# Performance work log

Measured on AMD Instinct MI355X. Metric: run time of the kernel, lower is better.

Reference implementation:

```python
import jax, jax.numpy as jnp
import numpy as np

N_NODES = 50000

def gcn_conv(x, W, b, row, col, ew, n):
    # PyG GCNConv: linear first (no bias in lin), then gcn_norm with added
    # self-loops (weight 1.0), symmetric D^{-1/2} normalization, scatter-add
    # aggregation from row (source) to col (target), then bias.
    h = x @ W                                      # [N, out]
    loop = jnp.arange(n, dtype=row.dtype)
    row_f = jnp.concatenate([row, loop])
    col_f = jnp.concatenate([col, loop])
    ew_f = jnp.concatenate([ew, jnp.ones((n,), dtype=ew.dtype)])
    deg = jax.ops.segment_sum(ew_f, col_f, num_segments=n)
    dinv = jnp.where(deg > 0, jax.lax.rsqrt(jnp.maximum(deg, 1e-30)), 0.0)
    norm = dinv[row_f] * ew_f * dinv[col_f]        # [E+N]
    msg = norm[:, None] * h[row_f]                 # gather + scale
    out = jax.ops.segment_sum(msg, col_f, num_segments=n)  # scatter-add
    return out + b

def setup_inputs() -> dict:
    key = jax.random.key(0)
    k = jax.random.split(key, 8)
    in_dim, hidden_dim, out_dim = 128, 256, 128
    n, e = N_NODES, 600000
    x = jax.random.normal(k[0], (n, in_dim), dtype=jnp.float32)
    edge_index = jax.random.randint(k[1], (2, e), 0, n, dtype=jnp.int64)
    edge_weight = jax.random.uniform(k[2], (e,), dtype=jnp.float32)
    # Glorot-style params (PyG GCNConv lin has no bias; bias added after aggregation)
    W1 = jax.random.normal(k[3], (in_dim, hidden_dim), dtype=jnp.float32) / np.sqrt(in_dim)
    b1 = jnp.zeros((hidden_dim,), dtype=jnp.float32)
    W2 = jax.random.normal(k[4], (hidden_dim, out_dim), dtype=jnp.float32) / np.sqrt(hidden_dim)
    b2 = jnp.zeros((out_dim,), dtype=jnp.float32)
    return {"x": x, "edge_index": edge_index, "edge_weight": edge_weight,
            "W1": W1, "b1": b1, "W2": W2, "b2": b2}

def reference(x, edge_index, edge_weight, W1, b1, W2, b2):
    n = x.shape[0]
    row, col = edge_index[0], edge_index[1]
    h = jax.nn.relu(gcn_conv(x, W1, b1, row, col, edge_weight, n))
    # dropout is identity in eval mode
    out = jax.nn.relu(gcn_conv(h, W2, b2, row, col, edge_weight, n))
    return out
```

## Files before the change

kernel.cpp:

```cpp
#include <hip/hip_runtime.h>
#include <hip/hip_bf16.h>

constexpr int IN_DIM  = 128;
constexpr int HID     = 256;
constexpr int OUT_DIM = 128;
constexpr int ELL_W   = 64;

typedef __attribute__((ext_vector_type(8))) short short8;
typedef __attribute__((ext_vector_type(8))) unsigned short ushort8;
typedef __attribute__((ext_vector_type(4))) float f32x4;

__device__ __forceinline__ float bf2f(unsigned short u) {
    return __uint_as_float(((unsigned int)u) << 16);
}
__device__ __forceinline__ unsigned short f2bf(float f) {
    unsigned int u = __float_as_uint(f);
    u += 0x7FFFu + ((u >> 16) & 1u);
    return (unsigned short)(u >> 16);
}
__device__ __forceinline__ unsigned short f2h(float f) {
    _Float16 h = (_Float16)f;
    unsigned short b;
    __builtin_memcpy(&b, &h, 2);
    return b;
}
__device__ __forceinline__ float h2f(unsigned short b) {
    _Float16 h;
    __builtin_memcpy(&h, &b, 2);
    return (float)h;
}
__device__ __forceinline__ unsigned int pack_e(int src, float w) {
    return (unsigned int)src | ((unsigned int)f2h(w) << 16);
}

__global__ void k_prep(int* __restrict__ cnt, int n,
                       const float* __restrict__ W1, unsigned short* __restrict__ w1t,
                       const float* __restrict__ W2, unsigned short* __restrict__ w2t) {
    const int i = blockIdx.x * 256 + threadIdx.x;
    if (i < n) cnt[i] = 0;
    if (i < IN_DIM * HID) {
        const int k = i / HID, nn = i % HID;
        w1t[(size_t)nn * IN_DIM + k] = f2bf(W1[i]);
    }
    if (i < HID * OUT_DIM) {
        const int k = i / OUT_DIM, nn = i % OUT_DIM;
        w2t[(size_t)nn * HID + k] = f2bf(W2[i]);
    }
}

__global__ void k_fill_ell(const int* __restrict__ row, const int* __restrict__ col,
                           const float* __restrict__ ew, int* __restrict__ cnt,
                           unsigned int* __restrict__ ell, int E) {
    const int e = blockIdx.x * blockDim.x + threadIdx.x;
    if (e < E) {
        const int c = col[e];
        const int p = atomicAdd(&cnt[c], 1);
        if (p < ELL_W)
            __builtin_nontemporal_store(pack_e(row[e], ew[e]), &ell[(size_t)c * ELL_W + p]);
    }
}

__global__ __launch_bounds__(256)
void k_deg_xs(const int* __restrict__ cnt, const unsigned int* __restrict__ ell,
              const float* __restrict__ x, float* __restrict__ dinv,
              unsigned short* __restrict__ xs, int n) {
    const int wave = threadIdx.x >> 6;
    const int lane = threadIdx.x & 63;
    const int node = blockIdx.x * 4 + wave;
    if (node >= n) return;
    const int m = min(cnt[node], ELL_W);
    float s = (lane < m) ? h2f((unsigned short)(ell[(size_t)node * ELL_W + lane] >> 16)) : 0.f;
    #pragma unroll
    for (int d = 32; d; d >>= 1) s += __shfl_xor(s, d);
    const float di = rsqrtf(1.0f + s);
    if (lane == 0) dinv[node] = di;
    const float2 v = *reinterpret_cast<const float2*>(x + (size_t)node * IN_DIM + lane * 2);
    const unsigned int packed = (unsigned int)f2bf(v.x * di) |
                                ((unsigned int)f2bf(v.y * di) << 16);
    *reinterpret_cast<unsigned int*>(xs + (size_t)node * IN_DIM + lane * 2) = packed;
}

template<bool BIAS_RELU, bool BF16OUT>
__global__ __launch_bounds__(256)
void k_gather_w(const int* __restrict__ cnt, const unsigned int* __restrict__ ell,
                const float* __restrict__ dinv, const unsigned short* __restrict__ hs,
                const float* __restrict__ bias, void* __restrict__ out_, int n) {
    constexpr int F = 128;
    const int gid  = threadIdx.x >> 4;
    const int gw   = gid & 3;
    const int l16  = threadIdx.x & 15;
    const int j8   = l16 * 8;
    const int node = blockIdx.x * 16 + gid;
    if (node >= n) return;

    const int m = min(cnt[node], ELL_W);
    const unsigned int* bucket = ell + (size_t)node * ELL_W;

    const float dc = dinv[node];
    const ushort8 hv = *reinterpret_cast<const ushort8*>(hs + (size_t)node * F + j8);

    float acc[8] = {};
    for (int base = 0; base < m; base += 16) {
        const unsigned int mt = (base + l16 < m) ? bucket[base + l16] : 0u;
        const int c16   = min(m - base, 16);
        const int quads = (c16 + 3) >> 2;
        unsigned int u[4];
        ushort8 v[4];
        #pragma unroll
        for (int i = 0; i < 4; ++i) {
            u[i] = __shfl(mt, gw * 16 + i);
            v[i] = *(const ushort8*)&hs[(size_t)(u[i] & 0xFFFFu) * F + j8];
        }
        for (int q = 1; q < quads; ++q) {
            unsigned int nu[4];
            ushort8 nv[4];
            #pragma unroll
            for (int i = 0; i < 4; ++i) {
                nu[i] = __shfl(mt, gw * 16 + q * 4 + i);
                nv[i] = *(const ushort8*)&hs[(size_t)(nu[i] & 0xFFFFu) * F + j8];
            }
            #pragma unroll
            for (int i = 0; i < 4; ++i) {
                const float f = h2f((unsigned short)(u[i] >> 16));
                #pragma unroll
                for (int k = 0; k < 8; ++k) acc[k] = fmaf(f, bf2f(v[i][k]), acc[k]);
            }
            #pragma unroll
            for (int i = 0; i < 4; ++i) { u[i] = nu[i]; v[i] = nv[i]; }
        }
        #pragma unroll
        for (int i = 0; i < 4; ++i) {
            const float f = h2f((unsigned short)(u[i] >> 16));
            #pragma unroll
            for (int k = 0; k < 8; ++k) acc[k] = fmaf(f, bf2f(v[i][k]), acc[k]);
        }
    }

    float o[8];
    if (BIAS_RELU) {
        const float4 b0 = *reinterpret_cast<const float4*>(bias + j8);
        const float4 b1 = *reinterpret_cast<const float4*>(bias + j8 + 4);
        const float bb[8] = {b0.x, b0.y, b0.z, b0.w, b1.x, b1.y, b1.z, b1.w};
        #pragma unroll
        for (int i = 0; i < 8; ++i)
            o[i] = fmaxf(fmaf(dc, acc[i] + bf2f(hv[i]), bb[i]), 0.f);
    } else {
        #pragma unroll
        for (int i = 0; i < 8; ++i) o[i] = dc * (acc[i] + bf2f(hv[i]));
    }
    if (BF16OUT) {
        unsigned short ob[8];
        #pragma unroll
        for (int i = 0; i < 8; ++i) ob[i] = f2bf(o[i]);
        *reinterpret_cast<uint4*>((unsigned short*)out_ + (size_t)node * F + j8) =
            *reinterpret_cast<uint4*>(ob);
    } else {
        float* op = (float*)out_ + (size_t)node * F + j8;
        *reinterpret_cast<float4*>(op)     = make_float4(o[0], o[1], o[2], o[3]);
        *reinterpret_cast<float4*>(op + 4) = make_float4(o[4], o[5], o[6], o[7]);
    }
}

__global__ __launch_bounds__(256, 2)
void k_gemm_fused(const unsigned short* __restrict__ A,
                  const unsigned short* __restrict__ W1t,
                  const unsigned short* __restrict__ W2t,
                  const float* __restrict__ b1,
                  const float* __restrict__ dinv,
                  unsigned short* __restrict__ H2,
                  int n, int tpb) {
    __shared__ unsigned short As[2][32 * 128];
    __shared__ unsigned short Hs[32 * 256];
    __shared__ unsigned short Os[32 * 128];

    const int t    = threadIdx.x;
    const int w    = t >> 6;
    const int lane = t & 63;
    const int quad = lane >> 4;
    const int l16  = lane & 15;
    const int xr   = (l16 & 7) << 3;

    short8 bw1[4][4];
    #pragma unroll
    for (int nt = 0; nt < 4; ++nt)
        #pragma unroll
        for (int ks = 0; ks < 4; ++ks)
            bw1[nt][ks] = *(const short8*)&W1t[(size_t)(w * 64 + nt * 16 + l16) * 128 + ks * 32 + quad * 8];
    short8 bw2[2][8];
    #pragma unroll
    for (int nt = 0; nt < 2; ++nt)
        #pragma unroll
        for (int ks = 0; ks < 8; ++ks)
            bw2[nt][ks] = *(const short8*)&W2t[(size_t)(w * 32 + nt * 16 + l16) * 256 + ks * 32 + quad * 8];
    float bv[4];
    #pragma unroll
    for (int nt = 0; nt < 4; ++nt) bv[nt] = b1[w * 64 + nt * 16 + l16];

    const int tile0 = blockIdx.x * tpb;

    auto stage = [&](int buf, int tile) {
        #pragma unroll
        for (int j = 0; j < 2; ++j) {
            const int ci = j * 256 + t;
            const int r  = ci >> 4;
            const int c  = (ci & 15) ^ (r & 7);
            __builtin_amdgcn_global_load_lds(
                (const __attribute__((address_space(1))) uint32_t*)(A + ((size_t)tile * 32 + r) * 128 + c * 8),
                (__attribute__((address_space(3))) uint32_t*)(&As[buf][ci * 8]), 16, 0, 0);
        }
    };

    stage(0, tile0);
    __syncthreads();

    for (int it = 0; it < tpb; ++it) {
        const int tile = tile0 + it;
        if (it + 1 < tpb) stage((it + 1) & 1, tile + 1);

        f32x4 acc1[2][4] = {};
        #pragma unroll
        for (int ks = 0; ks < 4; ++ks) {
            short8 af[2];
            #pragma unroll
            for (int mt = 0; mt < 2; ++mt)
                af[mt] = *(const short8*)&As[it & 1][(mt * 16 + l16) * 128 + ((ks * 32 + quad * 8) ^ xr)];
            #pragma unroll
            for (int mt = 0; mt < 2; ++mt)
                #pragma unroll
                for (int nt = 0; nt < 4; ++nt)
                    acc1[mt][nt] = __builtin_amdgcn_mfma_f32_16x16x32_bf16(
                        af[mt], bw1[nt][ks], acc1[mt][nt], 0, 0, 0);
        }
        __syncthreads();

        #pragma unroll
        for (int mt = 0; mt < 2; ++mt)
            #pragma unroll
            for (int i = 0; i < 4; ++i) {
                const int r  = mt * 16 + quad * 4 + i;
                const int xw = (r & 7) << 3;
                #pragma unroll
                for (int nt = 0; nt < 4; ++nt) {
                    const int col = w * 64 + nt * 16 + l16;
                    Hs[r * 256 + (col ^ xw)] = f2bf(fmaxf(acc1[mt][nt][i] + bv[nt], 0.f));
                }
            }
        __syncthreads();

        f32x4 acc2[2][2] = {};
        #pragma unroll
        for (int ks = 0; ks < 8; ++ks) {
            short8 af[2];
            #pragma unroll
            for (int mt = 0; mt < 2; ++mt)
                af[mt] = *(const short8*)&Hs[(mt * 16 + l16) * 256 + ((ks * 32 + quad * 8) ^ xr)];
            #pragma unroll
            for (int mt = 0; mt < 2; ++mt)
                #pragma unroll
                for (int nt = 0; nt < 2; ++nt)
                    acc2[mt][nt] = __builtin_amdgcn_mfma_f32_16x16x32_bf16(
                        af[mt], bw2[nt][ks], acc2[mt][nt], 0, 0, 0);
        }

        #pragma unroll
        for (int mt = 0; mt < 2; ++mt)
            #pragma unroll
            for (int i = 0; i < 4; ++i) {
                const int r  = mt * 16 + quad * 4 + i;
                const int rg = tile * 32 + r;
                const float dr = (rg < n) ? dinv[rg] : 0.f;
                const int xw = (r & 7) << 3;
                #pragma unroll
                for (int nt = 0; nt < 2; ++nt) {
                    const int col = w * 32 + nt * 16 + l16;
                    Os[r * 128 + (col ^ xw)] = f2bf(acc2[mt][nt][i] * dr);
                }
            }
        __syncthreads();

        #pragma unroll
        for (int j = 0; j < 2; ++j) {
            const int ci = j * 256 + t;
            const int r  = ci >> 4;
            const int cr = ci & 15;
            *(uint4*)&H2[((size_t)tile * 32 + r) * 128 + cr * 8] =
                *(const uint4*)&Os[r * 128 + ((cr ^ (r & 7)) * 8)];
        }
    }
}

extern "C" void kernel_launch(void* const* d_in, const int* in_sizes, int n_in,
                              void* d_out, int out_size, void* d_ws, size_t ws_size,
                              hipStream_t stream) {
    const float* x  = (const float*)d_in[0];
    const int*   ei = (const int*)d_in[1];
    const float* ew = (const float*)d_in[2];
    const float* W1 = (const float*)d_in[3];
    const float* b1 = (const float*)d_in[4];
    const float* W2 = (const float*)d_in[5];
    const float* b2 = (const float*)d_in[6];
    float* out = (float*)d_out;

    const int n = in_sizes[0] / IN_DIM;
    const int E = in_sizes[1] / 2;
    const int Mpad = (n + 127) & ~127;
    const int ntiles = Mpad / 32;
    const int TPB = 4;
    const int* row = ei;
    const int* col = ei + E;

    float* ws = (float*)d_ws;
    size_t o = 0;
    auto alloc = [&](size_t words) { float* p = ws + o; o += (words + 63) & ~(size_t)63; return p; };
    float* dinv = alloc(n);
    int*   cnt  = (int*)alloc(n);
    unsigned int* ell = (unsigned int*)alloc((size_t)n * ELL_W);
    unsigned short* xs   = (unsigned short*)alloc((size_t)Mpad * IN_DIM / 2);
    unsigned short* aggx = (unsigned short*)alloc((size_t)Mpad * IN_DIM / 2);
    unsigned short* h2s  = (unsigned short*)alloc((size_t)Mpad * OUT_DIM / 2);
    unsigned short* w1t  = (unsigned short*)alloc((size_t)IN_DIM * HID / 2);
    unsigned short* w2t  = (unsigned short*)alloc((size_t)HID * OUT_DIM / 2);

    k_prep<<<(n + 255) / 256, 256, 0, stream>>>(cnt, n, W1, w1t, W2, w2t);
    k_fill_ell<<<(E + 255) / 256, 256, 0, stream>>>(row, col, ew, cnt, ell, E);
    k_deg_xs<<<(n + 3) / 4, 256, 0, stream>>>(cnt, ell, x, dinv, xs, n);

    k_gather_w<false, true><<<(n + 15) / 16, 256, 0, stream>>>(cnt, ell, dinv, xs, nullptr, aggx, n);

    k_gemm_fused<<<ntiles / TPB, 256, 0, stream>>>(aggx, w1t, w2t, b1, dinv, h2s, n, TPB);

    k_gather_w<true, false><<<(n + 15) / 16, 256, 0, stream>>>(cnt, ell, dinv, h2s, b2, out, n);
}
```

Measured before the change: 205.7 us.

## Split gather feature dimension into four slices with cross-lane edge reduction

The gather kernel now launches four blocks per node chunk, each handling a 32-feature slice. Within a 16-lane group, the lanes split into four edge sub-groups of four lanes, so each lane loads 16 bytes of a different edge's row, followed by a shuffle reduction. The aim is to get more independent memory requests in flight and better L2 locality per slice, at the cost of re-reading each ELL bucket four times and doing extra shuffles. The bucket load is also made nontemporal, and the GEMM tiles-per-block drops from 4 to 2 to launch more blocks.

```diff
diff --git a/kernel.cpp b/kernel.cpp
--- a/kernel.cpp
+++ b/kernel.cpp
@@ -82,82 +82,76 @@
 
 template<bool BIAS_RELU, bool BF16OUT>
 __global__ __launch_bounds__(256)
-void k_gather_w(const int* __restrict__ cnt, const unsigned int* __restrict__ ell,
-                const float* __restrict__ dinv, const unsigned short* __restrict__ hs,
-                const float* __restrict__ bias, void* __restrict__ out_, int n) {
+void k_gather_sl(const int* __restrict__ cnt, const unsigned int* __restrict__ ell,
+                 const float* __restrict__ dinv, const unsigned short* __restrict__ hs,
+                 const float* __restrict__ bias, void* __restrict__ out_, int n) {
     constexpr int F = 128;
+    const int slice = blockIdx.x & 3;
+    const int chunk = blockIdx.x >> 2;
     const int gid  = threadIdx.x >> 4;
     const int gw   = gid & 3;
     const int l16  = threadIdx.x & 15;
-    const int j8   = l16 * 8;
-    const int node = blockIdx.x * 16 + gid;
+    const int node = chunk * 16 + gid;
     if (node >= n) return;
+
+    const int sl = slice * 32;
+    const int fq = (l16 & 3) * 8;
+    const int eo = l16 >> 2;
 
     const int m = min(cnt[node], ELL_W);
     const unsigned int* bucket = ell + (size_t)node * ELL_W;
-
     const float dc = dinv[node];
-    const ushort8 hv = *reinterpret_cast<const ushort8*>(hs + (size_t)node * F + j8);
 
     float acc[8] = {};
     for (int base = 0; base < m; base += 16) {
-        const unsigned int mt = (base + l16 < m) ? bucket[base + l16] : 0u;
-        const int c16   = min(m - base, 16);
-        const int quads = (c16 + 3) >> 2;
+        const unsigned int mt = (base + l16 < m) ?
+            __builtin_nontemporal_load(bucket + base + l16) : 0u;
         unsigned int u[4];
         ushort8 v[4];
         #pragma unroll
-        for (int i = 0; i < 4; ++i) {
-            u[i] = __shfl(mt, gw * 16 + i);
-            v[i] = *(const ushort8*)&hs[(size_t)(u[i] & 0xFFFFu) * F + j8];
-        }
-        for (int q = 1; q < quads; ++q) {
-            unsigned int nu[4];
-            ushort8 nv[4];
-            #pragma unroll
-            for (int i = 0; i < 4; ++i) {
-                nu[i] = __shfl(mt, gw * 16 + q * 4 + i);
-                nv[i] = *(const ushort8*)&hs[(size_t)(nu[i] & 0xFFFFu) * F + j8];
-            }
-            #pragma unroll
-            for (int i = 0; i < 4; ++i) {
-                const float f = h2f((unsigned short)(u[i] >> 16));
-                #pragma unroll
-                for (int k = 0; k < 8; ++k) acc[k] = fmaf(f, bf2f(v[i][k]), acc[k]);
-            }
-            #pragma unroll
-            for (int i = 0; i < 4; ++i) { u[i] = nu[i]; v[i] = nv[i]; }
-        }
-        #pragma unroll
-        for (int i = 0; i < 4; ++i) {
-            const float f = h2f((unsigned short)(u[i] >> 16));
-            #pragma unroll
-            for (int k = 0; k < 8; ++k) acc[k] = fmaf(f, bf2f(v[i][k]), acc[k]);
-        }
-    }
-
-    float o[8];
-    if (BIAS_RELU) {
-        const float4 b0 = *reinterpret_cast<const float4*>(bias + j8);
-        const float4 b1 = *reinterpret_cast<const float4*>(bias + j8 + 4);
-        const float bb[8] = {b0.x, b0.y, b0.z, b0.w, b1.x, b1.y, b1.z, b1.w};
-        #pragma unroll
-        for (int i = 0; i < 8; ++i)
-            o[i] = fmaxf(fmaf(dc, acc[i] + bf2f(hv[i]), bb[i]), 0.f);
-    } else {
-        #pragma unroll
-        for (int i = 0; i < 8; ++i) o[i] = dc * (acc[i] + bf2f(hv[i]));
-    }
-    if (BF16OUT) {
-        unsigned short ob[8];
-        #pragma unroll
-        for (int i = 0; i < 8; ++i) ob[i] = f2bf(o[i]);
-        *reinterpret_cast<uint4*>((unsigned short*)out_ + (size_t)node * F + j8) =
-            *reinterpret_cast<uint4*>(ob);
-    } else {
-        float* op = (float*)out_ + (size_t)node * F + j8;
-        *reinterpret_cast<float4*>(op)     = make_float4(o[0], o[1], o[2], o[3]);
-        *reinterpret_cast<float4*>(op + 4) = make_float4(o[4], o[5], o[6], o[7]);
+        for (int s = 0; s < 4; ++s) {
+            u[s] = __shfl(mt, gw * 16 + s * 4 + eo);
+            v[s] = *(const ushort8*)&hs[(size_t)(u[s] & 0xFFFFu) * F + sl + fq];
+        }
+        #pragma unroll
+        for (int s = 0; s < 4; ++s) {
+            const float f = h2f((unsigned short)(u[s] >> 16));
+            #pragma unroll
+            for (int k = 0; k < 8; ++k) acc[k] = fmaf(f, bf2f(v[s][k]), acc[k]);
+        }
+    }
+
+    #pragma unroll
+    for (int k = 0; k < 8; ++k) {
+        acc[k] += __shfl_xor(acc[k], 4);
+        acc[k] += __shfl_xor(acc[k], 8);
+    }
+
+    if (l16 < 4) {
+        const ushort8 hv = *(const ushort8*)&hs[(size_t)node * F + sl + l16 * 8];
+        float o[8];
+        if (BIAS_RELU) {
+            const float4 b0 = *(const float4*)&bias[sl + l16 * 8];
+            const float4 b1 = *(const float4*)&bias[sl + l16 * 8 + 4];
+            const float bb[8] = {b0.x, b0.y, b0.z, b0.w, b1.x, b1.y, b1.z, b1.w};
+            #pragma unroll
+            for (int k = 0; k < 8; ++k)
+                o[k] = fmaxf(fmaf(dc, acc[k] + bf2f(hv[k]), bb[k]), 0.f);
+        } else {
+            #pragma unroll
+            for (int k = 0; k < 8; ++k) o[k] = dc * (acc[k] + bf2f(hv[k]));
+        }
+        if (BF16OUT) {
+            unsigned short ob[8];
+            #pragma unroll
+            for (int k = 0; k < 8; ++k) ob[k] = f2bf(o[k]);
+            *reinterpret_cast<uint4*>((unsigned short*)out_ + (size_t)node * F + sl + l16 * 8) =
+                *reinterpret_cast<uint4*>(ob);
+        } else {
+            float* op = (float*)out_ + (size_t)node * F + sl + l16 * 8;
+            *reinterpret_cast<float4*>(op)     = make_float4(o[0], o[1], o[2], o[3]);
+            *reinterpret_cast<float4*>(op + 4) = make_float4(o[4], o[5], o[6], o[7]);
+        }
     }
 }
 
@@ -305,7 +299,7 @@
     const int E = in_sizes[1] / 2;
     const int Mpad = (n + 127) & ~127;
     const int ntiles = Mpad / 32;
-    const int TPB = 4;
+    const int TPB = 2;
     const int* row = ei;
     const int* col = ei + E;
 
@@ -321,13 +315,15 @@
     unsigned short* w1t  = (unsigned short*)alloc((size_t)IN_DIM * HID / 2);
     unsigned short* w2t  = (unsigned short*)alloc((size_t)HID * OUT_DIM / 2);
 
+    const int chunks = (n + 15) / 16;
+
     k_prep<<<(n + 255) / 256, 256, 0, stream>>>(cnt, n, W1, w1t, W2, w2t);
     k_fill_ell<<<(E + 255) / 256, 256, 0, stream>>>(row, col, ew, cnt, ell, E);
     k_deg_xs<<<(n + 3) / 4, 256, 0, stream>>>(cnt, ell, x, dinv, xs, n);
 
-    k_gather_w<false, true><<<(n + 15) / 16, 256, 0, stream>>>(cnt, ell, dinv, xs, nullptr, aggx, n);
+    k_gather_sl<false, true><<<chunks * 4, 256, 0, stream>>>(cnt, ell, dinv, xs, nullptr, aggx, n);
 
     k_gemm_fused<<<ntiles / TPB, 256, 0, stream>>>(aggx, w1t, w2t, b1, dinv, h2s, n, TPB);
 
-    k_gather_w<true, false><<<(n + 15) / 16, 256, 0, stream>>>(cnt, ell, dinv, h2s, b2, out, n);
-}
+    k_gather_sl<true, false><<<chunks * 4, 256, 0, stream>>>(cnt, ell, dinv, h2s, b2, out, n);
+}
```

After: 239.2 us. +16.3%, slower.
